# Kernel optimization log

Hardware: AMD Instinct MI355X
Metric: run time of the kernel (lower is better)

Reference implementation:

```python
import jax, jax.numpy as jnp
import numpy as np

EPS = 1e-5


def gcn_conv(x, W, b, src, dst):
    """PyG GCNConv: transform, add self-loops, symmetric norm, scatter-add, bias."""
    N = x.shape[0]
    h = x @ W  # [N, out]
    loop = jnp.arange(N)
    s = jnp.concatenate([src, loop])  # sources incl. self-loops
    d = jnp.concatenate([dst, loop])  # targets incl. self-loops
    deg = jax.ops.segment_sum(jnp.ones(s.shape[0], h.dtype), d, num_segments=N)
    dis = jnp.where(deg > 0, jax.lax.rsqrt(deg), 0.0)  # deg^-1/2
    norm = dis[s] * dis[d]  # [E+N]
    out = jax.ops.segment_sum(h[s] * norm[:, None], d, num_segments=N)
    return out + b


def batchnorm(x, gamma, beta):
    mu = x.mean(axis=0)
    var = x.var(axis=0)
    return (x - mu) * jax.lax.rsqrt(var + EPS) * gamma + beta


def setup_inputs() -> dict:
    key = jax.random.key(0)
    ks = jax.random.split(key, 6)
    N, E = 100000, 1600000
    IN, HID, OUT = 128, 256, 64
    x = jax.random.normal(ks[0], (N, IN), dtype=jnp.float32)
    edge_index = jax.random.randint(ks[1], (2, E), 0, N, dtype=jnp.int64)
    W1 = jax.random.normal(ks[2], (IN, HID), dtype=jnp.float32) / np.sqrt(IN)
    b1 = jnp.zeros((HID,), jnp.float32)
    gamma1 = jnp.ones((HID,), jnp.float32)
    beta1 = jnp.zeros((HID,), jnp.float32)
    W2 = jax.random.normal(ks[3], (HID, OUT), dtype=jnp.float32) / np.sqrt(HID)
    b2 = jnp.zeros((OUT,), jnp.float32)
    return {"x": x, "edge_index": edge_index, "W1": W1, "b1": b1,
            "gamma1": gamma1, "beta1": beta1, "W2": W2, "b2": b2}


def reference(x, edge_index, W1, b1, gamma1, beta1, W2, b2):
    src, dst = edge_index[0], edge_index[1]
    h = gcn_conv(x, W1, b1, src, dst)
    h = jax.nn.relu(batchnorm(h, gamma1, beta1))
    # dropout is identity at inference
    return gcn_conv(h, W2, b2, src, dst)
```

## Files before the change

kernel.cpp:

```cpp
#include <hip/hip_runtime.h>
#include <hip/hip_bf16.h>


#define IN_F  128
#define HID_F 256
#define OUT_F 64
#define BK_SHIFT 8
#define BK_SIZE  256
#define CHUNK    8192
#define CAP      8192

typedef unsigned int uint;
typedef unsigned short ushort;
typedef short bf16x8 __attribute__((ext_vector_type(8)));
typedef float f32x4 __attribute__((ext_vector_type(4)));

__device__ __forceinline__ ushort f2bf(float f) {
    uint u = __float_as_uint(f);
    uint r = (u + 0x7fffu + ((u >> 16) & 1u)) >> 16;
    return (ushort)r;
}
__device__ __forceinline__ float bf_lo(uint u) { return __uint_as_float(u << 16); }
__device__ __forceinline__ float bf_hi(uint u) { return __uint_as_float(u & 0xffff0000u); }

__device__ __forceinline__ void d2(float& a, uint u, uint m) {
    asm("v_dot2_f32_bf16 %0, %1, %2, %0" : "+v"(a) : "v"(u), "v"(m));
}

#define ACC8(u)                                                 \
    do {                                                        \
        d2(acc[0], (u).x, MLO); d2(acc[1], (u).x, MHI);         \
        d2(acc[2], (u).y, MLO); d2(acc[3], (u).y, MHI);         \
        d2(acc[4], (u).z, MLO); d2(acc[5], (u).z, MHI);         \
        d2(acc[6], (u).w, MLO); d2(acc[7], (u).w, MHI);         \
    } while (0)


__global__ __launch_bounds__(512) void scatter_wprep_kernel(
        const int* __restrict__ src, const int* __restrict__ dst,
        int* __restrict__ bcursor, uint* __restrict__ ebuf,
        const float* __restrict__ W1, const float* __restrict__ W2,
        ushort* __restrict__ W1bp, ushort* __restrict__ W2bp,
        int E, int NB, int nchunk) {
    if (blockIdx.x >= nchunk) {
        int i = (blockIdx.x - nchunk) * 512 + threadIdx.x;
        if (i < 32768) {
            int kk = i & 31, c = (i >> 5) & 255, kc = i >> 13;
            W1bp[i] = f2bf(W1[(size_t)(kc * 32 + kk) * HID_F + c]);
        } else {
            int j = i - 32768;
            int kk = j & 31, c = (j >> 5) & 63, kc = j >> 11;
            W2bp[j] = f2bf(W2[(size_t)(kc * 32 + kk) * OUT_F + c]);
        }
        return;
    }
    __shared__ int h[512];
    __shared__ int cur[512];
    for (int i = threadIdx.x; i < NB; i += 512) h[i] = 0;
    __syncthreads();
    int base = blockIdx.x * CHUNK;
    int end = min(base + CHUNK, E);
    for (int i = base + threadIdx.x; i < end; i += 512)
        atomicAdd(&h[dst[i] >> BK_SHIFT], 1);
    __syncthreads();
    for (int i = threadIdx.x; i < NB; i += 512)
        cur[i] = i * CAP + (h[i] ? atomicAdd(&bcursor[i], h[i]) : 0);
    __syncthreads();
    for (int i = base + threadIdx.x; i < end; i += 512) {
        int d = dst[i], s = src[i];
        int b = d >> BK_SHIFT;
        int pos = atomicAdd(&cur[b], 1);
        ebuf[pos] = (uint)s | ((uint)(d & (BK_SIZE - 1)) << 24);
    }
}

__global__ __launch_bounds__(1024) void bucket_build_kernel(
        const uint* __restrict__ ebuf, const int* __restrict__ bcursor,
        int* __restrict__ deg_e, int* __restrict__ offsets,
        float* __restrict__ dis, int* __restrict__ ssrc, int N) {
    __shared__ int cnt[256], off[256], cur[256];
    int b = blockIdx.x;
    int t = threadIdx.x;
    if (t < 256) cnt[t] = 0;
    __syncthreads();
    int e0 = b * CAP;
    int e1 = e0 + min(bcursor[b], CAP);
    for (int i = e0 + t; i < e1; i += 1024)
        atomicAdd(&cnt[ebuf[i] >> 24], 1);
    __syncthreads();
    int v = (t < 256) ? cnt[t] : 0;
    int vpad = (v + 3) & ~3;
    if (t < 256) off[t] = vpad;
    __syncthreads();
    for (int o = 1; o < 256; o <<= 1) {
        int u = (t >= o && t < 256) ? off[t - o] : 0;
        __syncthreads();
        if (t < 256) off[t] += u;
        __syncthreads();
    }
    int base_pad = b * (CAP + 768);
    if (t < 256) {
        int excl = off[t] - vpad;
        int d = b * BK_SIZE + t;
        if (d < N) {
            deg_e[d] = vpad;
            offsets[d] = base_pad + excl;
            dis[d] = rsqrtf((float)(v + 1));
        }
        cur[t] = excl;
    }
    __syncthreads();
    for (int i = e0 + t; i < e1; i += 1024) {
        uint e = ebuf[i];
        int ld = e >> 24;
        int pos = atomicAdd(&cur[ld], 1);
        ssrc[base_pad + pos] = (int)(e & 0xFFFFFFu);
    }
    __syncthreads();
    if (t < 256) {
        int excl = off[t] - vpad;
        for (int i = v; i < vpad; i++)
            ssrc[base_pad + excl + i] = N;
    }
}

__global__ void xprep_kernel(const float* __restrict__ x, const float* __restrict__ dis,
                             uint* __restrict__ xs, int N) {
    int i = blockIdx.x * 256 + threadIdx.x;
    if (i < (N + 1) * 32) {
        int n = i >> 5;
        if (n >= N) { ((uint2*)xs)[i] = make_uint2(0u, 0u); return; }
        float dn = dis[n];
        float4 v = ((const float4*)x)[i];
        uint2 o;
        o.x = (uint)f2bf(dn * v.x) | ((uint)f2bf(dn * v.y) << 16);
        o.y = (uint)f2bf(dn * v.z) | ((uint)f2bf(dn * v.w) << 16);
        ((uint2*)xs)[i] = o;
    }
}


__global__ void aggx_kernel(const uint* __restrict__ xs, const int* __restrict__ ssrc,
                            const int* __restrict__ offsets, const int* __restrict__ deg_e,
                            const float* __restrict__ dis, uint* __restrict__ zb, int N) {
    const uint MLO = 0x00003F80u, MHI = 0x3F800000u;
    int lane = threadIdx.x & 63;
    int half = lane >> 5;
    int hl = lane & 31;
    int grp = hl >> 3;
    int ck = hl & 7;
    int j = blockIdx.x & 7;
    int fo = (j >> 2) << 5;
    int oct = ((blockIdx.x >> 3) << 2) + (j & 3);
    int n = (oct << 3) + ((threadIdx.x >> 6) << 1) + half;
    if (n >= N) return;
    float acc[8];
#pragma unroll
    for (int i = 0; i < 8; i++) acc[i] = 0.f;
    int start = offsets[n], cnt = deg_e[n];
    uint4 uself = *(const uint4*)(xs + ((size_t)n << 6) + fo + (ck << 2));
    int hbase = half << 5;
    for (int base = 0; base < cnt; base += 32) {
        int m = min(32, cnt - base);
        int idx = base + hl;
        int sv = ssrc[start + (idx < cnt ? idx : cnt - 1)];
        int rounds = m >> 2;
        int q = 0;
        for (; q + 4 <= rounds; q += 4) {
            int sA = __shfl(sv, hbase | ((q + 0) << 2) | grp);
            int sB = __shfl(sv, hbase | ((q + 1) << 2) | grp);
            int sC = __shfl(sv, hbase | ((q + 2) << 2) | grp);
            int sD = __shfl(sv, hbase | ((q + 3) << 2) | grp);
            uint4 uA = *(const uint4*)(xs + ((size_t)sA << 6) + fo + (ck << 2));
            uint4 uB = *(const uint4*)(xs + ((size_t)sB << 6) + fo + (ck << 2));
            uint4 uC = *(const uint4*)(xs + ((size_t)sC << 6) + fo + (ck << 2));
            uint4 uD = *(const uint4*)(xs + ((size_t)sD << 6) + fo + (ck << 2));
            ACC8(uA); ACC8(uB); ACC8(uC); ACC8(uD);
        }
        for (; q < rounds; q++) {
            int s = __shfl(sv, hbase | (q << 2) | grp);
            uint4 u = *(const uint4*)(xs + ((size_t)s << 6) + fo + (ck << 2));
            ACC8(u);
        }
    }
#pragma unroll
    for (int i = 0; i < 8; i++) acc[i] += __shfl_down(acc[i], 16);
#pragma unroll
    for (int i = 0; i < 8; i++) acc[i] += __shfl_down(acc[i], 8);
    if (grp == 0) {
        ACC8(uself);
        float dn = dis[n];
        uint4 o;
        o.x = (uint)f2bf(dn * acc[0]) | ((uint)f2bf(dn * acc[1]) << 16);
        o.y = (uint)f2bf(dn * acc[2]) | ((uint)f2bf(dn * acc[3]) << 16);
        o.z = (uint)f2bf(dn * acc[4]) | ((uint)f2bf(dn * acc[5]) << 16);
        o.w = (uint)f2bf(dn * acc[6]) | ((uint)f2bf(dn * acc[7]) << 16);
        *(uint4*)(zb + ((size_t)n << 6) + fo + (ck << 2)) = o;
    }
}

__global__ __launch_bounds__(256) void gemm1_kernel(const uint* __restrict__ zb,
                                                    const uint* __restrict__ W1bp,
                                                    const float* __restrict__ b1,
                                                    ushort* __restrict__ out1b,
                                                    float* __restrict__ bnp, int N) {
    __shared__ uint sbuf[8192];
    int t = threadIdx.x;
    int n0 = blockIdx.x * 64;
    for (int i = t; i < 64 * 16; i += 256) {
        int r = i >> 4, q = i & 15;
        int node = n0 + r;
        uint4 v = make_uint4(0u, 0u, 0u, 0u);
        if (node < N) v = *(const uint4*)(zb + (size_t)node * 64 + q * 4);
        int p = q ^ (r & 15);
        *(uint4*)(&sbuf[r * 64 + p * 4]) = v;
    }
    __syncthreads();
    int wave = t >> 6, lane = t & 63;
    int quad = lane >> 4, lrow = lane & 15;
    f32x4 acc[4][4];
#pragma unroll
    for (int m = 0; m < 4; m++)
#pragma unroll
        for (int nt = 0; nt < 4; nt++) acc[m][nt] = (f32x4)(0.f);
#pragma unroll
    for (int kc = 0; kc < 4; kc++) {
        bf16x8 bfr[4];
#pragma unroll
        for (int nt = 0; nt < 4; nt++) {
            int c = wave * 64 + nt * 16 + lrow;
            bfr[nt] = *(const bf16x8*)(W1bp + ((size_t)(kc * 256 + c) * 16 + quad * 4));
        }
        bf16x8 afr[4];
#pragma unroll
        for (int m = 0; m < 4; m++) {
            int p = (kc * 4 + quad) ^ lrow;
            afr[m] = *(const bf16x8*)(&sbuf[(m * 16 + lrow) * 64 + p * 4]);
        }
#pragma unroll
        for (int m = 0; m < 4; m++)
#pragma unroll
            for (int nt = 0; nt < 4; nt++)
                acc[m][nt] = __builtin_amdgcn_mfma_f32_16x16x32_bf16(
                    afr[m], bfr[nt], acc[m][nt], 0, 0, 0);
    }
    __syncthreads();
#pragma unroll
    for (int nt = 0; nt < 4; nt++) {
        int c = wave * 64 + nt * 16 + lrow;
        float bb = b1[c];
        float s = 0.f, q = 0.f;
#pragma unroll
        for (int m = 0; m < 4; m++) {
#pragma unroll
            for (int r = 0; r < 4; r++) {
                int row = m * 16 + quad * 4 + r;
                float v = acc[m][nt][r] + bb;
                if (n0 + row < N) { s += v; q = fmaf(v, v, q); }
                uint hv = (uint)f2bf(v);
                uint pv = __shfl_xor(hv, 1);
                if ((lrow & 1) == 0)
                    sbuf[row * 128 + (c >> 1)] = hv | (pv << 16);
            }
        }
        s += __shfl_down(s, 32); q += __shfl_down(q, 32);
        s += __shfl_down(s, 16); q += __shfl_down(q, 16);
        if (quad == 0) {
            bnp[(size_t)blockIdx.x * 512 + c] = s;
            bnp[(size_t)blockIdx.x * 512 + 256 + c] = q;
        }
    }
    __syncthreads();
    uint* out1g = (uint*)out1b;
    for (int i = t; i < 2048; i += 256) {
        int row = i >> 5;
        if (n0 + row < N)
            *(uint4*)(out1g + (size_t)(n0 + row) * 128 + (i & 31) * 4) =
                *(const uint4*)(&sbuf[i * 4]);
    }
}

__global__ void bnred_kernel(const float* __restrict__ bnp, float* __restrict__ bnsum,
                             int nblk) {
    int g = blockIdx.x, t = threadIdx.x;
    float s = 0.f, q = 0.f;
    for (int b = g; b < nblk; b += 32) {
        s += bnp[(size_t)b * 512 + t];
        q += bnp[(size_t)b * 512 + 256 + t];
    }
    atomicAdd(&bnsum[t], s);
    atomicAdd(&bnsum[256 + t], q);
}

__global__ __launch_bounds__(256) void gemm2_kernel(const ushort* __restrict__ out1b,
                                                    const uint* __restrict__ W2bp,
                                                    const float* __restrict__ dis,
                                                    const float* __restrict__ bnsum,
                                                    const float* __restrict__ gamma,
                                                    const float* __restrict__ beta,
                                                    ushort* __restrict__ gs, int N) {
    __shared__ uint sbuf[8192];
    __shared__ float bns[256], bnb[256];
    const uint* out1u = (const uint*)out1b;
    int t = threadIdx.x;
    int n0 = blockIdx.x * 64;
    if (blockIdx.x == 0 && t < 32) ((uint*)gs)[(size_t)N * 32 + t] = 0u;
    {
        float invN = 1.0f / (float)N;
        float mean = bnsum[t] * invN;
        float var = bnsum[256 + t] * invN - mean * mean;
        float sc = gamma[t] * rsqrtf(fmaxf(var, 0.f) + 1e-5f);
        bns[t] = sc;
        bnb[t] = beta[t] - mean * sc;
    }
    __syncthreads();
    for (int i = t; i < 64 * 32; i += 256) {
        int r = i >> 5, q = i & 31;
        int node = n0 + r;
        uint4 v = make_uint4(0u, 0u, 0u, 0u);
        if (node < N) {
            uint4 w = *(const uint4*)(out1u + (size_t)node * 128 + q * 4);
            int c0 = q * 8;
            float r0 = fmaxf(fmaf(bf_lo(w.x), bns[c0 + 0], bnb[c0 + 0]), 0.f);
            float r1 = fmaxf(fmaf(bf_hi(w.x), bns[c0 + 1], bnb[c0 + 1]), 0.f);
            float r2 = fmaxf(fmaf(bf_lo(w.y), bns[c0 + 2], bnb[c0 + 2]), 0.f);
            float r3 = fmaxf(fmaf(bf_hi(w.y), bns[c0 + 3], bnb[c0 + 3]), 0.f);
            float r4 = fmaxf(fmaf(bf_lo(w.z), bns[c0 + 4], bnb[c0 + 4]), 0.f);
            float r5 = fmaxf(fmaf(bf_hi(w.z), bns[c0 + 5], bnb[c0 + 5]), 0.f);
            float r6 = fmaxf(fmaf(bf_lo(w.w), bns[c0 + 6], bnb[c0 + 6]), 0.f);
            float r7 = fmaxf(fmaf(bf_hi(w.w), bns[c0 + 7], bnb[c0 + 7]), 0.f);
            v.x = (uint)f2bf(r0) | ((uint)f2bf(r1) << 16);
            v.y = (uint)f2bf(r2) | ((uint)f2bf(r3) << 16);
            v.z = (uint)f2bf(r4) | ((uint)f2bf(r5) << 16);
            v.w = (uint)f2bf(r6) | ((uint)f2bf(r7) << 16);
        }
        int p = (q & 16) | ((q & 15) ^ (r & 15));
        *(uint4*)(&sbuf[r * 128 + p * 4]) = v;
    }
    __syncthreads();
    int wave = t >> 6, lane = t & 63;
    int quad = lane >> 4, lrow = lane & 15;
    int c = wave * 16 + lrow;
    f32x4 acc[4];
#pragma unroll
    for (int m = 0; m < 4; m++) acc[m] = (f32x4)(0.f);
#pragma unroll
    for (int kc = 0; kc < 8; kc++) {
        bf16x8 bfr = *(const bf16x8*)(W2bp + ((size_t)(kc * 64 + c) * 16 + quad * 4));
#pragma unroll
        for (int m = 0; m < 4; m++) {
            int q = kc * 4 + quad;
            int p = (q & 16) | ((q & 15) ^ lrow);
            bf16x8 afr = *(const bf16x8*)(&sbuf[(m * 16 + lrow) * 128 + p * 4]);
            acc[m] = __builtin_amdgcn_mfma_f32_16x16x32_bf16(afr, bfr, acc[m], 0, 0, 0);
        }
    }
    __syncthreads();
#pragma unroll
    for (int m = 0; m < 4; m++) {
#pragma unroll
        for (int r = 0; r < 4; r++) {
            int row = m * 16 + quad * 4 + r;
            int node = n0 + row;
            float dn = (node < N) ? dis[node] : 0.f;
            uint hv = (uint)f2bf(dn * acc[m][r]);
            uint pv = __shfl_xor(hv, 1);
            if ((lrow & 1) == 0)
                sbuf[row * 32 + (c >> 1)] = hv | (pv << 16);
        }
    }
    __syncthreads();
    uint* gsg = (uint*)gs;
    for (int i = t; i < 512; i += 256) {
        int row = i >> 3;
        if (n0 + row < N)
            *(uint4*)(gsg + (size_t)(n0 + row) * 32 + (i & 7) * 4) =
                *(const uint4*)(&sbuf[i * 4]);
    }
}

__global__ void agg2_kernel(const uint* __restrict__ gs, const int* __restrict__ ssrc,
                            const int* __restrict__ offsets, const int* __restrict__ deg_e,
                            const float* __restrict__ dis, const float* __restrict__ b2,
                            float* __restrict__ out, int N) {
    const uint MLO = 0x00003F80u, MHI = 0x3F800000u;
    int lane = threadIdx.x & 63;
    int half = lane >> 5;
    int hl = lane & 31;
    int grp = hl >> 3;
    int ck = hl & 7;
    int n = blockIdx.x * 8 + ((threadIdx.x >> 6) << 1) + half;
    if (n >= N) return;
    float acc[8];
#pragma unroll
    for (int i = 0; i < 8; i++) acc[i] = 0.f;
    int start = offsets[n], cnt = deg_e[n];
    int hbase = half << 5;
    for (int base = 0; base < cnt; base += 32) {
        int m = min(32, cnt - base);
        int idx = base + hl;
        int sv = ssrc[start + (idx < cnt ? idx : cnt - 1)];
        int rounds = m >> 2;
        int q = 0;
        for (; q + 2 <= rounds; q += 2) {
            int sA = __shfl(sv, hbase | ((q + 0) << 2) | grp);
            int sB = __shfl(sv, hbase | ((q + 1) << 2) | grp);
            uint4 uA = *(const uint4*)(gs + ((size_t)sA << 5) + (ck << 2));
            uint4 uB = *(const uint4*)(gs + ((size_t)sB << 5) + (ck << 2));
            ACC8(uA); ACC8(uB);
        }
        for (; q < rounds; q++) {
            int s = __shfl(sv, hbase | (q << 2) | grp);
            uint4 u = *(const uint4*)(gs + ((size_t)s << 5) + (ck << 2));
            ACC8(u);
        }
    }
#pragma unroll
    for (int i = 0; i < 8; i++) acc[i] += __shfl_down(acc[i], 16);
#pragma unroll
    for (int i = 0; i < 8; i++) acc[i] += __shfl_down(acc[i], 8);
    if (grp == 0) {
        uint4 u = *(const uint4*)(gs + ((size_t)n << 5) + (ck << 2));
        ACC8(u);
        float dn = dis[n];
        float4 bb0 = *(const float4*)(b2 + ck * 8);
        float4 bb1 = *(const float4*)(b2 + ck * 8 + 4);
        float* op = out + (size_t)n * OUT_F + ck * 8;
        *(float4*)op = make_float4(fmaf(dn, acc[0], bb0.x), fmaf(dn, acc[1], bb0.y),
                                   fmaf(dn, acc[2], bb0.z), fmaf(dn, acc[3], bb0.w));
        *(float4*)(op + 4) = make_float4(fmaf(dn, acc[4], bb1.x), fmaf(dn, acc[5], bb1.y),
                                         fmaf(dn, acc[6], bb1.z), fmaf(dn, acc[7], bb1.w));
    }
}

extern "C" void kernel_launch(void* const* d_in, const int* in_sizes, int n_in,
                              void* d_out, int out_size, void* d_ws, size_t ws_size,
                              hipStream_t stream) {
    const float* x      = (const float*)d_in[0];
    const int*   edges  = (const int*)d_in[1];
    const float* W1     = (const float*)d_in[2];
    const float* b1     = (const float*)d_in[3];
    const float* gamma1 = (const float*)d_in[4];
    const float* beta1  = (const float*)d_in[5];
    const float* W2     = (const float*)d_in[6];
    const float* b2     = (const float*)d_in[7];
    float* out = (float*)d_out;

    int N = in_sizes[0] / IN_F;
    int E = in_sizes[1] / 2;
    const int* src = edges;
    const int* dst = edges + E;
    int NB = (N + BK_SIZE - 1) / BK_SIZE;
    int nchunks = (E + CHUNK - 1) / CHUNK;
    int nblk1 = (N + 63) / 64;

    char* ws = (char*)d_ws;
    size_t off = 0;
    auto alloc = [&](size_t bytes) -> void* {
        void* p = ws + off;
        off += (bytes + 255) & ~(size_t)255;
        return p;
    };
    int*    deg_e   = (int*)alloc((size_t)N * 4);
    int*    offsets = (int*)alloc((size_t)N * 4);
    float*  dis     = (float*)alloc((size_t)(N + 1) * 4);
    int*    bcursor = (int*)alloc(512 * 4);
    float*  bnsum   = (float*)alloc(512 * 4);
    int*    ssrc    = (int*)alloc((size_t)NB * (CAP + 768) * 4);
    uint*   ebuf    = (uint*)alloc((size_t)NB * CAP * 4);
    uint*   xs      = (uint*)alloc((size_t)(N + 1) * (IN_F / 2) * 4);
    uint*   zb      = (uint*)alloc((size_t)N * (IN_F / 2) * 4);
    ushort* out1b   = (ushort*)alloc((size_t)N * HID_F * 2);
    float*  bnp     = (float*)alloc((size_t)nblk1 * 512 * 4);
    ushort* W1bp    = (ushort*)alloc(4 * 256 * 32 * 2);
    ushort* W2bp    = (ushort*)alloc(8 * 64 * 32 * 2);
    ushort* gs      = (ushort*)zb;

    hipMemsetAsync(bcursor, 0, 2 * 512 * 4, stream);

    scatter_wprep_kernel<<<nchunks + 96, 512, 0, stream>>>(src, dst, bcursor, ebuf,
                                                           W1, W2, W1bp, W2bp,
                                                           E, NB, nchunks);
    bucket_build_kernel<<<NB, 1024, 0, stream>>>(ebuf, bcursor, deg_e, offsets, dis, ssrc, N);
    xprep_kernel<<<((N + 1) * 32 + 255) / 256, 256, 0, stream>>>(x, dis, xs, N);
    {
        int noct = (N + 7) >> 3;
        int grid = ((noct + 3) >> 2) << 3;
        aggx_kernel<<<grid, 256, 0, stream>>>(xs, ssrc, offsets, deg_e, dis, zb, N);
    }
    gemm1_kernel<<<nblk1, 256, 0, stream>>>(zb, (const uint*)W1bp, b1, out1b, bnp, N);
    bnred_kernel<<<32, 256, 0, stream>>>(bnp, bnsum, nblk1);
    gemm2_kernel<<<nblk1, 256, 0, stream>>>(out1b, (const uint*)W2bp, dis, bnsum,
                                            gamma1, beta1, gs, N);
    agg2_kernel<<<(N + 7) / 8, 256, 0, stream>>>((const uint*)gs, ssrc, offsets, deg_e, dis,
                                                 b2, out, N);
}
```

Measured before the change: 316.0 us.

## Split bf16 feature table into 16-feature slices for aggregation locality

Rewrites xprep to store the scaled bf16 input features in eight feature-slice planes (16 features, 32 bytes per node each) instead of a row-major 256-byte row. Aggregation blocks now each handle one slice for a group of nodes, so the gathered working set per slice is smaller and more cache-resident. Each lane pair handles one neighbor, and padding lanes are redirected to the zero row. The cost is more blocks, more shuffle-reduction steps, smaller 16-byte gathers per edge, and a strided write pattern in xprep.

```diff
diff --git a/kernel.cpp b/kernel.cpp
--- a/kernel.cpp
+++ b/kernel.cpp
@@ -125,69 +125,71 @@
 }
 
 __global__ void xprep_kernel(const float* __restrict__ x, const float* __restrict__ dis,
-                             uint* __restrict__ xs, int N) {
+                             uint* __restrict__ xs2, int N) {
     int i = blockIdx.x * 256 + threadIdx.x;
     if (i < (N + 1) * 32) {
         int n = i >> 5;
-        if (n >= N) { ((uint2*)xs)[i] = make_uint2(0u, 0u); return; }
+        int q = i & 31;
+        int k = q >> 2;
+        int w = q & 3;
+        size_t oi = (size_t)k * (N + 1) * 4 + (size_t)n * 4 + w;
+        if (n >= N) { ((uint2*)xs2)[oi] = make_uint2(0u, 0u); return; }
         float dn = dis[n];
         float4 v = ((const float4*)x)[i];
         uint2 o;
         o.x = (uint)f2bf(dn * v.x) | ((uint)f2bf(dn * v.y) << 16);
         o.y = (uint)f2bf(dn * v.z) | ((uint)f2bf(dn * v.w) << 16);
-        ((uint2*)xs)[i] = o;
-    }
-}
-
-
-__global__ void aggx_kernel(const uint* __restrict__ xs, const int* __restrict__ ssrc,
+        ((uint2*)xs2)[oi] = o;
+    }
+}
+
+
+__global__ void aggx_kernel(const uint* __restrict__ xs2, const int* __restrict__ ssrc,
                             const int* __restrict__ offsets, const int* __restrict__ deg_e,
                             const float* __restrict__ dis, uint* __restrict__ zb, int N) {
     const uint MLO = 0x00003F80u, MHI = 0x3F800000u;
     int lane = threadIdx.x & 63;
     int half = lane >> 5;
     int hl = lane & 31;
-    int grp = hl >> 3;
-    int ck = hl & 7;
-    int j = blockIdx.x & 7;
-    int fo = (j >> 2) << 5;
-    int oct = ((blockIdx.x >> 3) << 2) + (j & 3);
+    int e = hl >> 1;
+    int so = (hl & 1) << 2;
+    int k = blockIdx.x & 7;
+    int oct = blockIdx.x >> 3;
     int n = (oct << 3) + ((threadIdx.x >> 6) << 1) + half;
     if (n >= N) return;
+    const uint* xsl = xs2 + (size_t)k * (N + 1) * 8;
     float acc[8];
 #pragma unroll
     for (int i = 0; i < 8; i++) acc[i] = 0.f;
     int start = offsets[n], cnt = deg_e[n];
-    uint4 uself = *(const uint4*)(xs + ((size_t)n << 6) + fo + (ck << 2));
+    uint4 uself = *(const uint4*)(xsl + ((size_t)n << 3) + so);
     int hbase = half << 5;
+    int i0 = hbase | e;
+    int i1 = i0 + 16;
     for (int base = 0; base < cnt; base += 32) {
-        int m = min(32, cnt - base);
         int idx = base + hl;
         int sv = ssrc[start + (idx < cnt ? idx : cnt - 1)];
-        int rounds = m >> 2;
-        int q = 0;
-        for (; q + 4 <= rounds; q += 4) {
-            int sA = __shfl(sv, hbase | ((q + 0) << 2) | grp);
-            int sB = __shfl(sv, hbase | ((q + 1) << 2) | grp);
-            int sC = __shfl(sv, hbase | ((q + 2) << 2) | grp);
-            int sD = __shfl(sv, hbase | ((q + 3) << 2) | grp);
-            uint4 uA = *(const uint4*)(xs + ((size_t)sA << 6) + fo + (ck << 2));
-            uint4 uB = *(const uint4*)(xs + ((size_t)sB << 6) + fo + (ck << 2));
-            uint4 uC = *(const uint4*)(xs + ((size_t)sC << 6) + fo + (ck << 2));
-            uint4 uD = *(const uint4*)(xs + ((size_t)sD << 6) + fo + (ck << 2));
-            ACC8(uA); ACC8(uB); ACC8(uC); ACC8(uD);
-        }
-        for (; q < rounds; q++) {
-            int s = __shfl(sv, hbase | (q << 2) | grp);
-            uint4 u = *(const uint4*)(xs + ((size_t)s << 6) + fo + (ck << 2));
-            ACC8(u);
+        int s0 = __shfl(sv, i0);
+        int s1 = __shfl(sv, i1);
+        if (base + e >= cnt) s0 = N;
+        uint4 uA = *(const uint4*)(xsl + ((size_t)s0 << 3) + so);
+        if (base + 16 < cnt) {
+            if (base + 16 + e >= cnt) s1 = N;
+            uint4 uB = *(const uint4*)(xsl + ((size_t)s1 << 3) + so);
+            ACC8(uA); ACC8(uB);
+        } else {
+            ACC8(uA);
         }
     }
 #pragma unroll
     for (int i = 0; i < 8; i++) acc[i] += __shfl_down(acc[i], 16);
 #pragma unroll
     for (int i = 0; i < 8; i++) acc[i] += __shfl_down(acc[i], 8);
-    if (grp == 0) {
+#pragma unroll
+    for (int i = 0; i < 8; i++) acc[i] += __shfl_down(acc[i], 4);
+#pragma unroll
+    for (int i = 0; i < 8; i++) acc[i] += __shfl_down(acc[i], 2);
+    if (hl < 2) {
         ACC8(uself);
         float dn = dis[n];
         uint4 o;
@@ -195,7 +197,7 @@
         o.y = (uint)f2bf(dn * acc[2]) | ((uint)f2bf(dn * acc[3]) << 16);
         o.z = (uint)f2bf(dn * acc[4]) | ((uint)f2bf(dn * acc[5]) << 16);
         o.w = (uint)f2bf(dn * acc[6]) | ((uint)f2bf(dn * acc[7]) << 16);
-        *(uint4*)(zb + ((size_t)n << 6) + fo + (ck << 2)) = o;
+        *(uint4*)(zb + ((size_t)n << 6) + (k << 3) + so) = o;
     }
 }
 
@@ -485,8 +487,7 @@
     xprep_kernel<<<((N + 1) * 32 + 255) / 256, 256, 0, stream>>>(x, dis, xs, N);
     {
         int noct = (N + 7) >> 3;
-        int grid = ((noct + 3) >> 2) << 3;
-        aggx_kernel<<<grid, 256, 0, stream>>>(xs, ssrc, offsets, deg_e, dis, zb, N);
+        aggx_kernel<<<noct << 3, 256, 0, stream>>>(xs, ssrc, offsets, deg_e, dis, zb, N);
     }
     gemm1_kernel<<<nblk1, 256, 0, stream>>>(zb, (const uint*)W1bp, b1, out1b, bnp, N);
     bnred_kernel<<<32, 256, 0, stream>>>(bnp, bnsum, nblk1);
```

New measurement: 410.8 us. 1.3x slower.
